# Optimization experiments

Measured on AMD Instinct MI355X. Metric: run time of the kernel, lower is better.

The kernel has to match this reference:

```python
import jax, jax.numpy as jnp
import numpy as np

N = 200000   # nodes
E = 500000   # edges
B = 4096     # batch of events
K = 20       # temporal neighbors
M = 100000   # pending raw messages
D = 128      # node feat / embedding dim
DT = 128     # time encoding dim (= D in TGN)
DM = 128     # memory dim
MSG = 128    # message dim
RAW = 2 * DM + D + DT   # 512 raw message dim
HID = RAW // 2          # 256 mlp hidden
HEADS = 2
QD = D + DT             # 256 attention query dim (= MHA embed_dim)
KD = D + DT + D         # 384 attention key dim (neigh feat + time + edge feat)
DH = QD // HEADS


def setup_inputs() -> dict:
    key = jax.random.key(0)
    ks = jax.random.split(key, 40)
    f = lambda i, shape, s=0.05: jax.random.normal(ks[i], shape, jnp.float32) * s
    ri = lambda i, shape, hi: jax.random.randint(ks[i], shape, 0, hi, jnp.int32)
    return {
        # event batch (int constants)
        'src_nodes': ri(0, (B,), N), 'dst_nodes': ri(1, (B,), N), 'neg_nodes': ri(2, (B,), N),
        'edge_times': ri(3, (B,), 1000000),
        # temporal neighbor lists for the 3B query nodes (neighbor_finder output)
        'neighbors': ri(4, (3 * B, K), N),
        'neighbor_edge_idxs': ri(5, (3 * B, K), E),
        'neighbor_edge_times': ri(6, (3 * B, K), 1000000),
        # pending raw message events ('last' aggregator picks last per node)
        'msg_src': ri(7, (M,), N), 'msg_dst': ri(8, (M,), N),
        'msg_eidx': ri(9, (M,), E), 'msg_t': ri(10, (M,), 1000000),
        'last_update': ri(11, (N,), 500000),
        # learned params / state (floats)
        'node_feats': f(12, (N, D)), 'edge_feats': f(13, (E, D)), 'memory': f(14, (N, DM)),
        'time_w': f(15, (DT,), 1.0), 'time_b': f(16, (DT,), 1.0),
        'msg_W1': f(17, (HID, RAW)), 'msg_b1': f(18, (HID,)),
        'msg_W2': f(19, (MSG, HID)), 'msg_b2': f(20, (MSG,)),
        'gru_Wi': f(21, (3 * DM, MSG)), 'gru_Wh': f(22, (3 * DM, DM)),
        'gru_bi': f(23, (3 * DM,)), 'gru_bh': f(24, (3 * DM,)),
        'Wq': f(25, (QD, QD)), 'bq': f(26, (QD,)),
        'Wk': f(27, (QD, KD)), 'bk': f(28, (QD,)),
        'Wv': f(29, (QD, KD)), 'bv': f(30, (QD,)),
        'Wo': f(31, (QD, QD)), 'bo': f(32, (QD,)),
        'mW1': f(33, (D, QD + D)), 'mb1': f(34, (D,)),
        'mW2': f(35, (D, D)), 'mb2': f(36, (D,)),
    }


def _time_enc(t, w, b):
    # TimeEncode: cos(t * w + b); t [...], out [..., DT]
    return jnp.cos(t[..., None] * w + b)


def _forward(node_feats, edge_feats, memory, time_w, time_b,
             msg_W1, msg_b1, msg_W2, msg_b2,
             gru_Wi, gru_Wh, gru_bi, gru_bh,
             Wq, bq, Wk, bk, Wv, bv, Wo, bo, mW1, mb1, mW2, mb2,
             src_nodes, dst_nodes, neg_nodes, edge_times,
             neighbors, neighbor_edge_idxs, neighbor_edge_times,
             msg_src, msg_dst, msg_eidx, msg_t, last_update):
    # ---- 1. get_updated_memory: 'last' aggregator + mlp message fn + GRU ----
    pos = jnp.arange(M, dtype=jnp.int32)
    last_pos = jnp.full((N,), -1, jnp.int32).at[msg_src].max(pos)  # last msg per node
    has_msg = last_pos >= 0
    idx = jnp.maximum(last_pos, 0)
    s, d = msg_src[idx], msg_dst[idx]
    e, t = msg_eidx[idx], msg_t[idx]
    dt = (t - last_update[s]).astype(jnp.float32)
    raw = jnp.concatenate([memory[s], memory[d], edge_feats[e],
                           _time_enc(dt, time_w, time_b)], axis=-1)  # [N, RAW]
    h1 = jax.nn.relu(raw @ msg_W1.T + msg_b1)
    msg = h1 @ msg_W2.T + msg_b2                                    # [N, MSG]
    # torch GRUCell (gate order r, z, n)
    gi = msg @ gru_Wi.T + gru_bi
    gh = memory @ gru_Wh.T + gru_bh
    ir, iz, inn = jnp.split(gi, 3, axis=-1)
    hr, hz, hn = jnp.split(gh, 3, axis=-1)
    r = jax.nn.sigmoid(ir + hr)
    z = jax.nn.sigmoid(iz + hz)
    n = jnp.tanh(inn + r * hn)
    new_mem = (1.0 - z) * n + z * memory
    mem_upd = jnp.where(has_msg[:, None], new_mem, memory)          # [N, DM]

    # ---- 2. graph-attention embedding (1 layer) over temporal neighbors ----
    nodes = jnp.concatenate([src_nodes, dst_nodes, neg_nodes])      # [3B]
    ts = jnp.tile(edge_times, 3).astype(jnp.float32)                # [3B]
    src_feat = mem_upd[nodes] + node_feats[nodes]                   # [3B, D]
    q_in = jnp.concatenate([src_feat,
                            _time_enc(jnp.zeros_like(ts), time_w, time_b)], -1)  # [3B, QD]
    pad_mask = neighbors == 0                                       # TGN: id 0 = padding
    n_feat = mem_upd[neighbors] + node_feats[neighbors]             # [3B, K, D]
    dt_n = ts[:, None] - neighbor_edge_times.astype(jnp.float32)
    k_in = jnp.concatenate([n_feat, _time_enc(dt_n, time_w, time_b),
                            edge_feats[neighbor_edge_idxs]], -1)    # [3B, K, KD]
    q = (q_in @ Wq.T + bq).reshape(-1, HEADS, DH)                   # [3B, H, DH]
    k = (k_in @ Wk.T + bk).reshape(-1, K, HEADS, DH)
    v = (k_in @ Wv.T + bv).reshape(-1, K, HEADS, DH)
    scores = jnp.einsum('bhd,bkhd->bhk', q, k) / jnp.sqrt(jnp.float32(DH))
    scores = jnp.where(pad_mask[:, None, :], -1e9, scores)
    attn = jax.nn.softmax(scores, axis=-1)                          # [3B, H, K]
    ctx = jnp.einsum('bhk,bkhd->bhd', attn, v).reshape(-1, QD)
    attn_out = ctx @ Wo.T + bo                                      # [3B, QD]
    all_masked = jnp.all(pad_mask, axis=-1)
    attn_out = jnp.where(all_masked[:, None], 0.0, attn_out)
    # MergeLayer(attn_out, src_feat)
    h = jax.nn.relu(jnp.concatenate([attn_out, src_feat], -1) @ mW1.T + mb1)
    emb = h @ mW2.T + mb2                                           # [3B, D]
    return emb.reshape(3, B, D)  # (source, destination, negative) embeddings


def reference(src_nodes, dst_nodes, neg_nodes, edge_times, neighbors,
              neighbor_edge_idxs, neighbor_edge_times, msg_src, msg_dst,
              msg_eidx, msg_t, last_update, node_feats, edge_feats, memory,
              time_w, time_b, msg_W1, msg_b1, msg_W2, msg_b2, gru_Wi, gru_Wh,
              gru_bi, gru_bh, Wq, bq, Wk, bk, Wv, bv, Wo, bo, mW1, mb1, mW2, mb2):
    return _forward(node_feats, edge_feats, memory, time_w, time_b,
                    msg_W1, msg_b1, msg_W2, msg_b2,
                    gru_Wi, gru_Wh, gru_bi, gru_bh,
                    Wq, bq, Wk, bk, Wv, bv, Wo, bo, mW1, mb1, mW2, mb2,
                    src_nodes, dst_nodes, neg_nodes, edge_times,
                    neighbors, neighbor_edge_idxs, neighbor_edge_times,
                    msg_src, msg_dst, msg_eidx, msg_t, last_update)
```

## Files before the change

kernel.cpp:

```cpp
#include <hip/hip_runtime.h>
#include <math.h>

#define NN 200000
#define EEDGE 500000
#define BB 4096
#define KK 20
#define MM 100000
#define Q3 (3*BB)
#define NBLK ((NN + 255) / 256)

typedef _Float16 __attribute__((ext_vector_type(8))) f16x8;
typedef _Float16 __attribute__((ext_vector_type(4))) f16x4;
typedef float __attribute__((ext_vector_type(4))) f32x4;

#define MFMA16(a,b,c) __builtin_amdgcn_mfma_f32_16x16x32_f16(a,b,c,0,0,0)

__device__ __forceinline__ float fast_cos(float a) {
    double ad = (double)a * 0.15915494309189535;
    double fr = ad - floor(ad);
    return __builtin_amdgcn_cosf((float)fr);
}

__device__ __forceinline__ float tenc(float dt, float w, float b) {
    float p = __fmul_rn(dt, w);
    float a = __fadd_rn(p, b);
    return fast_cos(a);
}

__device__ __forceinline__ float fsigm(float x) {
    return __builtin_amdgcn_rcpf(1.f + __expf(-x));
}
__device__ __forceinline__ float ftanh(float x) {
    return 1.f - 2.f * __builtin_amdgcn_rcpf(1.f + __expf(2.f * x));
}

__device__ __forceinline__ f32x4 z4() {
    f32x4 v; v[0] = 0.f; v[1] = 0.f; v[2] = 0.f; v[3] = 0.f; return v;
}

__global__ void k_init(int* lastpos, int* inv, char* mask) {
    int i = blockIdx.x * 256 + threadIdx.x;
    if (i < NN) { lastpos[i] = -1; inv[i] = -1; mask[i] = 0; }
}

__global__ void k_scatter(const int* __restrict__ msg_src, int* __restrict__ lastpos) {
    int i = blockIdx.x * 256 + threadIdx.x;
    if (i < MM) atomicMax(&lastpos[msg_src[i]], i);
}

__global__ void k_mark(const int* __restrict__ src_nodes, const int* __restrict__ dst_nodes,
                       const int* __restrict__ neg_nodes, const int* __restrict__ neighbors,
                       char* __restrict__ mask) {
    int i = blockIdx.x * 256 + threadIdx.x;
    if (i < Q3) {
        int node = (i < BB) ? src_nodes[i] : (i < 2 * BB) ? dst_nodes[i - BB] : neg_nodes[i - 2 * BB];
        mask[node] = 1;
    } else {
        int e = i - Q3;
        if (e < Q3 * KK) mask[neighbors[e]] = 1;
    }
}

__global__ void k_count(const int* __restrict__ lastpos, int* __restrict__ bcnt) {
    int n = blockIdx.x * 256 + threadIdx.x;
    int flag = (n < NN && lastpos[n] >= 0) ? 1 : 0;
    unsigned long long m = __ballot(flag != 0);
    __shared__ int wc[4];
    int wave = threadIdx.x >> 6, lane = threadIdx.x & 63;
    if (lane == 0) wc[wave] = __popcll(m);
    __syncthreads();
    if (threadIdx.x == 0) bcnt[blockIdx.x] = wc[0] + wc[1] + wc[2] + wc[3];
}

__global__ void k_scan(const int* __restrict__ bcnt, int* __restrict__ boff,
                       int* __restrict__ count) {
    __shared__ int s[NBLK];
    int t = threadIdx.x;
    for (int i = t; i < NBLK; i += 256) s[i] = bcnt[i];
    __syncthreads();
    if (t == 0) {
        int acc = 0;
        for (int i = 0; i < NBLK; i++) { int v = s[i]; s[i] = acc; acc += v; }
        *count = acc;
    }
    __syncthreads();
    for (int i = t; i < NBLK; i += 256) boff[i] = s[i];
}

__global__ void k_fill(const int* __restrict__ lastpos, const int* __restrict__ boff,
                       int* __restrict__ comp, int* __restrict__ inv) {
    int n = blockIdx.x * 256 + threadIdx.x;
    int flag = (n < NN && lastpos[n] >= 0) ? 1 : 0;
    unsigned long long m = __ballot(flag != 0);
    __shared__ int wc[4];
    int wave = threadIdx.x >> 6, lane = threadIdx.x & 63;
    if (lane == 0) wc[wave] = __popcll(m);
    __syncthreads();
    int base = boff[blockIdx.x];
    for (int i = 0; i < wave; i++) base += wc[i];
    int rank = __popcll(m & ((1ull << lane) - 1));
    if (flag) {
        int pos = base + rank;
        comp[pos] = n;
        inv[n] = pos;
    }
}

__global__ void k_prep(const float* __restrict__ Wq, const float* __restrict__ bq,
                       const float* __restrict__ time_b, float* __restrict__ bq2) {
    __shared__ float cte[128];
    int t = threadIdx.x;
    if (t < 128) cte[t] = fast_cos(time_b[t]);
    __syncthreads();
    float acc = bq[t];
    #pragma unroll 4
    for (int d = 0; d < 128; d++)
        acc += Wq[(size_t)t * 256 + 128 + d] * cte[d];
    bq2[t] = acc;
}

__global__ void k_cvtw(const float* __restrict__ W1, const float* __restrict__ W2,
                       const float* __restrict__ Wi, const float* __restrict__ Wh,
                       const float* __restrict__ Wq, const float* __restrict__ Wv,
                       const float* __restrict__ Wo, const float* __restrict__ mW1,
                       const float* __restrict__ mW2, const float* __restrict__ Wk,
                       _Float16* __restrict__ dst) {
    int f = blockIdx.x * 256 + threadIdx.x;
    if (f >= 77824) return;
    const float* src; int dstoff, K, ldb, lf, tr = -1;
    if      (f < 16384) { src = W1;  dstoff = 0;      K = 512; ldb = 512; lf = f; }
    else if (f < 20480) { src = W2;  dstoff = 131072; K = 256; ldb = 256; lf = f - 16384; }
    else if (f < 26624) { src = Wi;  dstoff = 163840; K = 128; ldb = 128; lf = f - 20480; }
    else if (f < 32768) { src = Wh;  dstoff = 212992; K = 128; ldb = 128; lf = f - 26624; }
    else if (f < 36864) { src = Wq;  dstoff = 262144; K = 128; ldb = 256; lf = f - 32768; }
    else if (f < 43008) { src = Wv;  dstoff = 294912; K = 384; ldb = 384; lf = f - 36864; }
    else if (f < 49152) { src = Wv + 128 * 384; dstoff = 344064; K = 384; ldb = 384; lf = f - 43008; }
    else if (f < 57344) { src = Wo;  dstoff = 393216; K = 256; ldb = 256; lf = f - 49152; }
    else if (f < 63488) { src = mW1; dstoff = 458752; K = 384; ldb = 384; lf = f - 57344; }
    else if (f < 65536) { src = mW2; dstoff = 507904; K = 128; ldb = 128; lf = f - 63488; }
    else if (f < 71680) { src = Wk;  dstoff = 524288; K = 128; ldb = 0; lf = f - 65536; tr = 0; }
    else                { src = Wk;  dstoff = 573440; K = 128; ldb = 0; lf = f - 71680; tr = 1; }
    int KS = K >> 5;
    int cgrp = lf / (KS * 64);
    int rem  = lf - cgrp * (KS * 64);
    int ks = rem >> 6, lane = rem & 63;
    int kg = lane >> 4, arow = lane & 15;
    int col = cgrp * 16 + arow;
    int k0 = ks * 32 + kg * 8;
    f16x8 h;
    if (tr < 0) {
        const float* p = src + (size_t)col * ldb + k0;
        float4 a = *(const float4*)p;
        float4 b = *(const float4*)(p + 4);
        h[0] = (_Float16)a.x; h[1] = (_Float16)a.y; h[2] = (_Float16)a.z; h[3] = (_Float16)a.w;
        h[4] = (_Float16)b.x; h[5] = (_Float16)b.y; h[6] = (_Float16)b.z; h[7] = (_Float16)b.w;
    } else {
        #pragma unroll
        for (int e = 0; e < 8; e++)
            h[e] = (_Float16)Wk[(size_t)(tr * 128 + k0 + e) * 384 + col];
    }
    *(f16x8*)(dst + dstoff + (size_t)lf * 8) = h;
}

__device__ __forceinline__ int SWA(int r, int byteofs) {
    return r * 1024 + (byteofs ^ ((r & 7) << 4));
}

__device__ __forceinline__ f16x8 ldw4(const _Float16* W, int cg, int ks, int lane) {
    return *(const f16x8*)(W + (((size_t)cg * 4 + ks) * 64 + lane) * 8);
}

__global__ __launch_bounds__(512, 2)
void k_stage1(const int* __restrict__ comp, const int* __restrict__ count,
              const int* __restrict__ lastpos,
              const int* __restrict__ msg_dst, const int* __restrict__ msg_eidx,
              const int* __restrict__ msg_t, const int* __restrict__ last_update,
              const float* __restrict__ memory, const float* __restrict__ edge_feats,
              const float* __restrict__ time_w, const float* __restrict__ time_b,
              const _Float16* __restrict__ W1h, const float* __restrict__ b1,
              const _Float16* __restrict__ W2h, const float* __restrict__ b2,
              const _Float16* __restrict__ Wih, const _Float16* __restrict__ Whh,
              const float* __restrict__ bi, const float* __restrict__ bh,
              _Float16* __restrict__ new_mem)
{
    __shared__ char rawb[64 * 1024];
    __shared__ int sn[64], sd[64], se[64];
    __shared__ float sdt[64];

    int cnt = *count;
    int r0 = blockIdx.x * 64;
    if (r0 >= cnt) return;
    int tid = threadIdx.x;

    if (tid < 64) {
        int rr = r0 + tid;
        int j = (rr < cnt) ? rr : r0;
        int n = comp[j];
        int idx = lastpos[n];
        sn[tid] = n;
        sd[tid] = msg_dst[idx];
        se[tid] = msg_eidx[idx];
        sdt[tid] = (float)(msg_t[idx] - last_update[n]);
    }
    __syncthreads();

    #pragma unroll
    for (int it = 0; it < 6; it++) {
        int gi = tid + it * 512;
        int r = gi / 48, g = gi - r * 48;
        const float* src;
        if (g < 16)      src = memory + (size_t)sn[r] * 128 + g * 8;
        else if (g < 32) src = memory + (size_t)sd[r] * 128 + (g - 16) * 8;
        else             src = edge_feats + (size_t)se[r] * 128 + (g - 32) * 8;
        float4 a = *(const float4*)src;
        float4 b = *(const float4*)(src + 4);
        f16x8 h;
        h[0] = (_Float16)a.x; h[1] = (_Float16)a.y; h[2] = (_Float16)a.z; h[3] = (_Float16)a.w;
        h[4] = (_Float16)b.x; h[5] = (_Float16)b.y; h[6] = (_Float16)b.z; h[7] = (_Float16)b.w;
        *(f16x8*)(rawb + SWA(r, g * 16)) = h;
    }
    #pragma unroll
    for (int it = 0; it < 2; it++) {
        int gi = tid + it * 512;
        int r = gi >> 4, g = gi & 15;
        int c = g * 8;
        float dt = sdt[r];
        float4 w0 = *(const float4*)(time_w + c);
        float4 w1 = *(const float4*)(time_w + c + 4);
        float4 t0 = *(const float4*)(time_b + c);
        float4 t1 = *(const float4*)(time_b + c + 4);
        f16x8 h;
        h[0] = (_Float16)tenc(dt, w0.x, t0.x); h[1] = (_Float16)tenc(dt, w0.y, t0.y);
        h[2] = (_Float16)tenc(dt, w0.z, t0.z); h[3] = (_Float16)tenc(dt, w0.w, t0.w);
        h[4] = (_Float16)tenc(dt, w1.x, t1.x); h[5] = (_Float16)tenc(dt, w1.y, t1.y);
        h[6] = (_Float16)tenc(dt, w1.z, t1.z); h[7] = (_Float16)tenc(dt, w1.w, t1.w);
        *(f16x8*)(rawb + SWA(r, (48 + g) * 16)) = h;
    }
    __syncthreads();

    int wv = tid >> 6, lane = tid & 63;
    int arow = lane & 15, kg = lane >> 4;

    f32x4 acc1[2][4];
    #pragma unroll
    for (int c = 0; c < 2; c++)
        #pragma unroll
        for (int rt = 0; rt < 4; rt++) acc1[c][rt] = z4();
    for (int ks = 0; ks < 16; ks++) {
        f16x8 a[4];
        #pragma unroll
        for (int rt = 0; rt < 4; rt++)
            a[rt] = *(const f16x8*)(rawb + SWA(rt * 16 + arow, ks * 64 + kg * 16));
        #pragma unroll
        for (int c = 0; c < 2; c++) {
            f16x8 b = *(const f16x8*)(W1h + (((size_t)(wv * 2 + c) * 16 + ks) * 64 + lane) * 8);
            #pragma unroll
            for (int rt = 0; rt < 4; rt++)
                acc1[c][rt] = MFMA16(a[rt], b, acc1[c][rt]);
        }
    }
    __syncthreads();

    #pragma unroll
    for (int c = 0; c < 2; c++) {
        int col = (wv * 2 + c) * 16 + arow;
        float bb = b1[col];
        #pragma unroll
        for (int rt = 0; rt < 4; rt++)
            #pragma unroll
            for (int rg = 0; rg < 4; rg++) {
                int row = rt * 16 + kg * 4 + rg;
                float v = fmaxf(acc1[c][rt][rg] + bb, 0.f);
                *(_Float16*)(rawb + SWA(row, 384 + col * 2)) = (_Float16)v;
            }
    }
    __syncthreads();

    f32x4 acc2[4];
    #pragma unroll
    for (int rt = 0; rt < 4; rt++) acc2[rt] = z4();
    for (int ks = 0; ks < 8; ks++) {
        f16x8 b = *(const f16x8*)(W2h + (((size_t)wv * 8 + ks) * 64 + lane) * 8);
        #pragma unroll
        for (int rt = 0; rt < 4; rt++) {
            f16x8 a = *(const f16x8*)(rawb + SWA(rt * 16 + arow, 384 + ks * 64 + kg * 16));
            acc2[rt] = MFMA16(a, b, acc2[rt]);
        }
    }
    __syncthreads();

    {
        int col = wv * 16 + arow;
        float bb = b2[col];
        #pragma unroll
        for (int rt = 0; rt < 4; rt++)
            #pragma unroll
            for (int rg = 0; rg < 4; rg++) {
                int row = rt * 16 + kg * 4 + rg;
                *(_Float16*)(rawb + SWA(row, 384 + col * 2)) =
                    (_Float16)(acc2[rt][rg] + bb);
            }
    }
    __syncthreads();

    f32x4 aR[4], aZ[4], aNi[4], aNh[4];
    #pragma unroll
    for (int rt = 0; rt < 4; rt++) { aR[rt] = z4(); aZ[rt] = z4(); aNi[rt] = z4(); aNh[rt] = z4(); }
    for (int ks = 0; ks < 4; ks++) {
        f16x8 bi_ = ldw4(Wih, wv, ks, lane);
        f16x8 bh_ = ldw4(Whh, wv, ks, lane);
        #pragma unroll
        for (int rt = 0; rt < 4; rt++) {
            f16x8 m = *(const f16x8*)(rawb + SWA(rt * 16 + arow, 384 + ks * 64 + kg * 16));
            f16x8 hh = *(const f16x8*)(rawb + SWA(rt * 16 + arow, ks * 64 + kg * 16));
            aR[rt] = MFMA16(m, bi_, aR[rt]);
            aR[rt] = MFMA16(hh, bh_, aR[rt]);
        }
    }
    for (int ks = 0; ks < 4; ks++) {
        f16x8 bi_ = ldw4(Wih, 8 + wv, ks, lane);
        f16x8 bh_ = ldw4(Whh, 8 + wv, ks, lane);
        #pragma unroll
        for (int rt = 0; rt < 4; rt++) {
            f16x8 m = *(const f16x8*)(rawb + SWA(rt * 16 + arow, 384 + ks * 64 + kg * 16));
            f16x8 hh = *(const f16x8*)(rawb + SWA(rt * 16 + arow, ks * 64 + kg * 16));
            aZ[rt] = MFMA16(m, bi_, aZ[rt]);
            aZ[rt] = MFMA16(hh, bh_, aZ[rt]);
        }
    }
    for (int ks = 0; ks < 4; ks++) {
        f16x8 bi_ = ldw4(Wih, 16 + wv, ks, lane);
        f16x8 bh_ = ldw4(Whh, 16 + wv, ks, lane);
        #pragma unroll
        for (int rt = 0; rt < 4; rt++) {
            f16x8 m = *(const f16x8*)(rawb + SWA(rt * 16 + arow, 384 + ks * 64 + kg * 16));
            f16x8 hh = *(const f16x8*)(rawb + SWA(rt * 16 + arow, ks * 64 + kg * 16));
            aNi[rt] = MFMA16(m, bi_, aNi[rt]);
            aNh[rt] = MFMA16(hh, bh_, aNh[rt]);
        }
    }

    {
        int col = wv * 16 + arow;
        float bir = bi[col],        bhr = bh[col];
        float biz = bi[128 + col],  bhz = bh[128 + col];
        float bin_ = bi[256 + col], bhn_ = bh[256 + col];
        #pragma unroll
        for (int rt = 0; rt < 4; rt++)
            #pragma unroll
            for (int rg = 0; rg < 4; rg++) {
                int row = rt * 16 + kg * 4 + rg;
                int rr = r0 + row;
                if (rr < cnt) {
                    float r_ = fsigm(aR[rt][rg] + bir + bhr);
                    float zg = fsigm(aZ[rt][rg] + biz + bhz);
                    float ng = ftanh(aNi[rt][rg] + bin_ + r_ * (aNh[rt][rg] + bhn_));
                    float om = (float)*(const _Float16*)(rawb + SWA(row, col * 2));
                    new_mem[(size_t)rr * 128 + col] = (_Float16)((1.f - zg) * ng + zg * om);
                }
            }
    }
}

__global__ __launch_bounds__(256)
void k_feat(const int* __restrict__ inv, const char* __restrict__ mask,
            const _Float16* __restrict__ new_mem,
            const float* __restrict__ memory, const float* __restrict__ node_feats,
            _Float16* __restrict__ feat)
{
    int idx = blockIdx.x * 256 + threadIdx.x;
    if (idx >= NN * 16) return;
    int n = idx >> 4, g = idx & 15;
    if (!mask[n]) return;
    int c = g * 8;
    int iv = inv[n];
    float4 n0 = *(const float4*)(node_feats + (size_t)n * 128 + c);
    float4 n1 = *(const float4*)(node_feats + (size_t)n * 128 + c + 4);
    f16x8 o;
    if (iv >= 0) {
        f16x8 mv = *(const f16x8*)(new_mem + (size_t)iv * 128 + c);
        o[0] = (_Float16)((float)mv[0] + n0.x); o[1] = (_Float16)((float)mv[1] + n0.y);
        o[2] = (_Float16)((float)mv[2] + n0.z); o[3] = (_Float16)((float)mv[3] + n0.w);
        o[4] = (_Float16)((float)mv[4] + n1.x); o[5] = (_Float16)((float)mv[5] + n1.y);
        o[6] = (_Float16)((float)mv[6] + n1.z); o[7] = (_Float16)((float)mv[7] + n1.w);
    } else {
        float4 m0 = *(const float4*)(memory + (size_t)n * 128 + c);
        float4 m1 = *(const float4*)(memory + (size_t)n * 128 + c + 4);
        o[0] = (_Float16)(m0.x + n0.x); o[1] = (_Float16)(m0.y + n0.y);
        o[2] = (_Float16)(m0.z + n0.z); o[3] = (_Float16)(m0.w + n0.w);
        o[4] = (_Float16)(m1.x + n1.x); o[5] = (_Float16)(m1.y + n1.y);
        o[6] = (_Float16)(m1.z + n1.z); o[7] = (_Float16)(m1.w + n1.w);
    }
    *(f16x8*)(feat + (size_t)n * 128 + c) = o;
}

__global__ __launch_bounds__(512, 2)
void k2b(const int* __restrict__ src_nodes, const int* __restrict__ dst_nodes,
         const int* __restrict__ neg_nodes, const _Float16* __restrict__ feat,
         const _Float16* __restrict__ WqLh, const float* __restrict__ bq2,
         const _Float16* __restrict__ Wkth,
         _Float16* __restrict__ sfeat, _Float16* __restrict__ qk_ws)
{
    __shared__ char lds[24 * 1024];
    __shared__ int snode[32];
    int tid = threadIdx.x;
    int r0 = blockIdx.x * 32;

    if (tid < 32) {
        int q = r0 + tid;
        snode[tid] = (q < BB) ? src_nodes[q] : (q < 2 * BB) ? dst_nodes[q - BB] : neg_nodes[q - 2 * BB];
    }
    __syncthreads();

    {
        int r = tid >> 4, g = tid & 15;
        f16x8 v = *(const f16x8*)(feat + (size_t)snode[r] * 128 + g * 8);
        *(f16x8*)(&lds[r * 256 + ((g * 16) ^ ((r & 7) << 4))]) = v;
        *(f16x8*)(sfeat + (size_t)(r0 + r) * 128 + g * 8) = v;
    }
    __syncthreads();

    int wv = tid >> 6, lane = tid & 63;
    int arow = lane & 15, kg = lane >> 4;

    f32x4 acc[2][2];
    #pragma unroll
    for (int c = 0; c < 2; c++) { acc[c][0] = z4(); acc[c][1] = z4(); }
    for (int ks = 0; ks < 4; ks++) {
        f16x8 a0 = *(const f16x8*)(&lds[arow * 256 + ((ks * 64 + kg * 16) ^ ((arow & 7) << 4))]);
        f16x8 a1 = *(const f16x8*)(&lds[(16 + arow) * 256 + ((ks * 64 + kg * 16) ^ ((arow & 7) << 4))]);
        #pragma unroll
        for (int c = 0; c < 2; c++) {
            f16x8 b = *(const f16x8*)(WqLh + (((size_t)(wv * 2 + c) * 4 + ks) * 64 + lane) * 8);
            acc[c][0] = MFMA16(a0, b, acc[c][0]);
            acc[c][1] = MFMA16(a1, b, acc[c][1]);
        }
    }
    #pragma unroll
    for (int c = 0; c < 2; c++) {
        int col = (wv * 2 + c) * 16 + arow;
        float bb = bq2[col];
        #pragma unroll
        for (int rt = 0; rt < 2; rt++)
            #pragma unroll
            for (int rg = 0; rg < 4; rg++) {
                int row = rt * 16 + kg * 4 + rg;
                *(_Float16*)(&lds[8192 + row * 512 + ((col * 2) ^ ((row & 7) << 4))]) =
                    (_Float16)(acc[c][rt][rg] + bb);
            }
    }
    __syncthreads();

    int h = wv >> 2;
    f32x4 acc2[6][2];
    #pragma unroll
    for (int c = 0; c < 6; c++) { acc2[c][0] = z4(); acc2[c][1] = z4(); }
    for (int ks = 0; ks < 4; ks++) {
        f16x8 a0 = *(const f16x8*)(&lds[8192 + arow * 512 +
                    ((h * 256 + ks * 64 + kg * 16) ^ ((arow & 7) << 4))]);
        f16x8 a1 = *(const f16x8*)(&lds[8192 + (16 + arow) * 512 +
                    ((h * 256 + ks * 64 + kg * 16) ^ ((arow & 7) << 4))]);
        #pragma unroll
        for (int c = 0; c < 6; c++) {
            int cgh = (wv & 3) * 6 + c;
            f16x8 b = *(const f16x8*)(Wkth + (size_t)h * 49152 +
                       (((size_t)cgh * 4 + ks) * 64 + lane) * 8);
            acc2[c][0] = MFMA16(a0, b, acc2[c][0]);
            acc2[c][1] = MFMA16(a1, b, acc2[c][1]);
        }
    }
    #pragma unroll
    for (int c = 0; c < 6; c++) {
        int cgh = (wv & 3) * 6 + c;
        int col = h * 384 + cgh * 16 + arow;
        #pragma unroll
        for (int rt = 0; rt < 2; rt++)
            #pragma unroll
            for (int rg = 0; rg < 4; rg++) {
                int row = rt * 16 + kg * 4 + rg;
                qk_ws[(size_t)(r0 + row) * 768 + col] = (_Float16)acc2[c][rt][rg];
            }
    }
}

template<int KD, int NFRAG, bool RELU>
__global__ __launch_bounds__(256, 4)
void k_gemm(const _Float16* __restrict__ A, int lda, int a_ys,
            const _Float16* __restrict__ B, int b_ys,
            const float* __restrict__ bias, int bias_ys,
            _Float16* __restrict__ C, int ldc, int c_ys,
            float* __restrict__ C32,
            const int* __restrict__ rowmask)
{
    constexpr int ROWB = KD * 2;
    __shared__ char As[32 * ROWB];
    int tid = threadIdx.x;
    int r0 = blockIdx.x * 32;
    int aoff = blockIdx.y * a_ys;
    const _Float16* Bp = B + (size_t)blockIdx.y * b_ys;
    int coff = blockIdx.y * c_ys;

    #pragma unroll
    for (int t = 0; t < (32 * KD / 8) / 256; t++) {
        int gi = tid + t * 256;
        int r = gi / (KD / 8), g = gi % (KD / 8);
        f16x8 v = *(const f16x8*)(A + (size_t)(r0 + r) * lda + aoff + g * 8);
        *(f16x8*)(&As[r * ROWB + ((g * 16) ^ ((r & 7) << 4))]) = v;
    }
    __syncthreads();

    int wv = tid >> 6, lane = tid & 63;
    int arow = lane & 15, kg = lane >> 4;
    f32x4 acc[NFRAG][2];
    #pragma unroll
    for (int c = 0; c < NFRAG; c++) { acc[c][0] = z4(); acc[c][1] = z4(); }

    #pragma unroll
    for (int ks = 0; ks < KD / 32; ks++) {
        f16x8 a0 = *(const f16x8*)(&As[arow * ROWB + ((ks * 64 + kg * 16) ^ ((arow & 7) << 4))]);
        f16x8 a1 = *(const f16x8*)(&As[(16 + arow) * ROWB + ((ks * 64 + kg * 16) ^ ((arow & 7) << 4))]);
        #pragma unroll
        for (int c = 0; c < NFRAG; c++) {
            f16x8 b = *(const f16x8*)(Bp +
                (((size_t)(wv * NFRAG + c) * (KD / 32) + ks) * 64 + lane) * 8);
            acc[c][0] = MFMA16(a0, b, acc[c][0]);
            acc[c][1] = MFMA16(a1, b, acc[c][1]);
        }
    }

    #pragma unroll
    for (int c = 0; c < NFRAG; c++) {
        int cg = (wv * NFRAG + c) * 16 + arow;
        float bb = bias ? bias[blockIdx.y * bias_ys + cg] : 0.f;
        #pragma unroll
        for (int rt = 0; rt < 2; rt++)
            #pragma unroll
            for (int rg = 0; rg < 4; rg++) {
                int grow = r0 + rt * 16 + kg * 4 + rg;
                float v = acc[c][rt][rg] + bb;
                if (RELU) v = fmaxf(v, 0.f);
                if (rowmask && rowmask[grow]) v = 0.f;
                if (C)   C[(size_t)grow * ldc + coff + cg] = (_Float16)v;
                if (C32) C32[(size_t)grow * ldc + coff + cg] = v;
            }
    }
}

__global__ __launch_bounds__(256)
void k2d(const int* __restrict__ neighbors, const int* __restrict__ nb_eidx,
         const int* __restrict__ nb_et, const int* __restrict__ edge_times,
         const _Float16* __restrict__ feat,
         const float* __restrict__ edge_feats, const float* __restrict__ time_w,
         const float* __restrict__ time_b,
         _Float16* __restrict__ qk_wsum, int* __restrict__ allm)
{
    int tid = threadIdx.x;
    int qi = blockIdx.x * 4 + (tid >> 6);
    int lane = tid & 63;
    int h = lane >> 5, l32 = lane & 31;
    int c0 = l32 * 4;

    float4 tw = *(const float4*)(time_w + c0);
    float4 tb = *(const float4*)(time_b + c0);

    const _Float16* qkp = qk_wsum + (size_t)qi * 768 + h * 384;
    f16x4 t0 = *(const f16x4*)(qkp + c0);
    f16x4 t1 = *(const f16x4*)(qkp + 128 + c0);
    f16x4 t2 = *(const f16x4*)(qkp + 256 + c0);
    float qk0[4], qk1[4], qk2[4];
    #pragma unroll
    for (int t = 0; t < 4; t++) { qk0[t] = (float)t0[t]; qk1[t] = (float)t1[t]; qk2[t] = (float)t2[t]; }

    float ts = (float)edge_times[qi & (BB - 1)];
    float m_run = -3.0e38f, l_run = 0.f;
    float w0[4] = {0,0,0,0}, w1[4] = {0,0,0,0}, w2[4] = {0,0,0,0};
    int anyv = 0;
    const float inv_sqrt = 0.08838834764831845f;

    int base = qi * KK;
    int nb_c = neighbors[base];
    int ei_c = nb_eidx[base];
    int et_c = nb_et[base];
    f16x4 fv;
    float4 ef;
    {
        fv = *(const f16x4*)(feat + (size_t)nb_c * 128 + c0);
        ef = *(const float4*)(edge_feats + (size_t)ei_c * 128 + c0);
    }

    for (int j = 0; j < KK; j++) {
        int nb_n = 0, ei_n = 0, et_n = 0;
        f16x4 fv_n = {0,0,0,0};
        float4 ef_n = {0,0,0,0};
        if (j + 1 < KK) {
            nb_n = neighbors[base + j + 1];
            ei_n = nb_eidx[base + j + 1];
            et_n = nb_et[base + j + 1];
            fv_n = *(const f16x4*)(feat + (size_t)nb_n * 128 + c0);
            ef_n = *(const float4*)(edge_feats + (size_t)ei_n * 128 + c0);
        }

        float dtf = ts - (float)et_c;
        anyv |= (nb_c != 0);
        float k0[4] = { (float)fv[0], (float)fv[1], (float)fv[2], (float)fv[3] };
        float k1[4] = { tenc(dtf, tw.x, tb.x), tenc(dtf, tw.y, tb.y),
                        tenc(dtf, tw.z, tb.z), tenc(dtf, tw.w, tb.w) };
        float k2[4] = { ef.x, ef.y, ef.z, ef.w };

        float sp = 0.f;
        #pragma unroll
        for (int t = 0; t < 4; t++)
            sp += qk0[t] * k0[t] + qk1[t] * k1[t] + qk2[t] * k2[t];
        sp += __shfl_xor(sp, 1, 32);
        sp += __shfl_xor(sp, 2, 32);
        sp += __shfl_xor(sp, 4, 32);
        sp += __shfl_xor(sp, 8, 32);
        sp += __shfl_xor(sp, 16, 32);

        float s = sp * inv_sqrt;
        if (nb_c == 0) s = -1e9f;
        float m_new = fmaxf(m_run, s);
        float sc = __expf(m_run - m_new);
        float p = __expf(s - m_new);
        l_run = l_run * sc + p;
        #pragma unroll
        for (int t = 0; t < 4; t++) {
            w0[t] = w0[t] * sc + p * k0[t];
            w1[t] = w1[t] * sc + p * k1[t];
            w2[t] = w2[t] * sc + p * k2[t];
        }
        m_run = m_new;

        nb_c = nb_n; ei_c = ei_n; et_c = et_n;
        fv = fv_n; ef = ef_n;
    }

    float linv = __builtin_amdgcn_rcpf(l_run);
    _Float16* wp = qk_wsum + (size_t)qi * 768 + h * 384;
    f16x4 o0, o1, o2;
    #pragma unroll
    for (int t = 0; t < 4; t++) {
        o0[t] = (_Float16)(w0[t] * linv);
        o1[t] = (_Float16)(w1[t] * linv);
        o2[t] = (_Float16)(w2[t] * linv);
    }
    *(f16x4*)(wp + c0) = o0;
    *(f16x4*)(wp + 128 + c0) = o1;
    *(f16x4*)(wp + 256 + c0) = o2;
    if (lane == 0) allm[qi] = anyv ? 0 : 1;
}

__global__ __launch_bounds__(256, 2)
void k2t2(const _Float16* __restrict__ ctx, const _Float16* __restrict__ sfeat,
          const _Float16* __restrict__ Woh, const float* __restrict__ bo,
          const _Float16* __restrict__ mW1h, const float* __restrict__ mb1,
          const _Float16* __restrict__ mW2h, const float* __restrict__ mb2,
          const int* __restrict__ allm, float* __restrict__ out)
{
    __shared__ char lds[48 * 1024];
    int tid = threadIdx.x;
    int r0 = blockIdx.x * 32;

    #pragma unroll
    for (int t = 0; t < 4; t++) {
        int gi = tid + t * 256;
        int r = gi >> 5, g = gi & 31;
        f16x8 v = *(const f16x8*)(ctx + (size_t)(r0 + r) * 256 + g * 8);
        *(f16x8*)(&lds[r * 512 + ((g * 16) ^ ((r & 7) << 4))]) = v;
    }
    __syncthreads();

    int wv = tid >> 6, lane = tid & 63;
    int arow = lane & 15, kg = lane >> 4;

    f32x4 acc[4][2];
    #pragma unroll
    for (int c = 0; c < 4; c++) { acc[c][0] = z4(); acc[c][1] = z4(); }
    for (int ks = 0; ks < 8; ks++) {
        f16x8 a0 = *(const f16x8*)(&lds[arow * 512 + ((ks * 64 + kg * 16) ^ ((arow & 7) << 4))]);
        f16x8 a1 = *(const f16x8*)(&lds[(16 + arow) * 512 + ((ks * 64 + kg * 16) ^ ((arow & 7) << 4))]);
        #pragma unroll
        for (int c = 0; c < 4; c++) {
            f16x8 b = *(const f16x8*)(Woh + (((size_t)(wv * 4 + c) * 8 + ks) * 64 + lane) * 8);
            acc[c][0] = MFMA16(a0, b, acc[c][0]);
            acc[c][1] = MFMA16(a1, b, acc[c][1]);
        }
    }
    #pragma unroll
    for (int c = 0; c < 4; c++) {
        int col = (wv * 4 + c) * 16 + arow;
        float bb = bo[col];
        #pragma unroll
        for (int rt = 0; rt < 2; rt++)
            #pragma unroll
            for (int rg = 0; rg < 4; rg++) {
                int row = rt * 16 + kg * 4 + rg;
                float v = allm[r0 + row] ? 0.f : (acc[c][rt][rg] + bb);
                *(_Float16*)(&lds[16384 + row * 768 + ((col * 2) ^ ((row & 7) << 4))]) = (_Float16)v;
            }
    }
    #pragma unroll
    for (int t = 0; t < 2; t++) {
        int gi = tid + t * 256;
        int r = gi >> 4, g = gi & 15;
        f16x8 v = *(const f16x8*)(sfeat + (size_t)(r0 + r) * 128 + g * 8);
        *(f16x8*)(&lds[16384 + r * 768 + ((512 + g * 16) ^ ((r & 7) << 4))]) = v;
    }
    __syncthreads();

    f32x4 acc2[2][2];
    #pragma unroll
    for (int c = 0; c < 2; c++) { acc2[c][0] = z4(); acc2[c][1] = z4(); }
    for (int ks = 0; ks < 12; ks++) {
        f16x8 a0 = *(const f16x8*)(&lds[16384 + arow * 768 + ((ks * 64 + kg * 16) ^ ((arow & 7) << 4))]);
        f16x8 a1 = *(const f16x8*)(&lds[16384 + (16 + arow) * 768 + ((ks * 64 + kg * 16) ^ ((arow & 7) << 4))]);
        #pragma unroll
        for (int c = 0; c < 2; c++) {
            f16x8 b = *(const f16x8*)(mW1h + (((size_t)(wv * 2 + c) * 12 + ks) * 64 + lane) * 8);
            acc2[c][0] = MFMA16(a0, b, acc2[c][0]);
            acc2[c][1] = MFMA16(a1, b, acc2[c][1]);
        }
    }
    #pragma unroll
    for (int c = 0; c < 2; c++) {
        int col = (wv * 2 + c) * 16 + arow;
        float bb = mb1[col];
        #pragma unroll
        for (int rt = 0; rt < 2; rt++)
            #pragma unroll
            for (int rg = 0; rg < 4; rg++) {
                int row = rt * 16 + kg * 4 + rg;
                float v = fmaxf(acc2[c][rt][rg] + bb, 0.f);
                *(_Float16*)(&lds[40960 + row * 256 + ((col * 2) ^ ((row & 7) << 4))]) = (_Float16)v;
            }
    }
    __syncthreads();

    f32x4 acc3[2][2];
    #pragma unroll
    for (int c = 0; c < 2; c++) { acc3[c][0] = z4(); acc3[c][1] = z4(); }
    for (int ks = 0; ks < 4; ks++) {
        f16x8 a0 = *(const f16x8*)(&lds[40960 + arow * 256 + ((ks * 64 + kg * 16) ^ ((arow & 7) << 4))]);
        f16x8 a1 = *(const f16x8*)(&lds[40960 + (16 + arow) * 256 + ((ks * 64 + kg * 16) ^ ((arow & 7) << 4))]);
        #pragma unroll
        for (int c = 0; c < 2; c++) {
            f16x8 b = *(const f16x8*)(mW2h + (((size_t)(wv * 2 + c) * 4 + ks) * 64 + lane) * 8);
            acc3[c][0] = MFMA16(a0, b, acc3[c][0]);
            acc3[c][1] = MFMA16(a1, b, acc3[c][1]);
        }
    }
    #pragma unroll
    for (int c = 0; c < 2; c++) {
        int col = (wv * 2 + c) * 16 + arow;
        float bb = mb2[col];
        #pragma unroll
        for (int rt = 0; rt < 2; rt++)
            #pragma unroll
            for (int rg = 0; rg < 4; rg++) {
                int row = rt * 16 + kg * 4 + rg;
                out[(size_t)(r0 + row) * 128 + col] = acc3[c][rt][rg] + bb;
            }
    }
}

extern "C" void kernel_launch(void* const* d_in, const int* in_sizes, int n_in,
                              void* d_out, int out_size, void* d_ws, size_t ws_size,
                              hipStream_t stream) {
    (void)in_sizes; (void)n_in; (void)out_size; (void)ws_size;
    const int* src_nodes  = (const int*)d_in[0];
    const int* dst_nodes  = (const int*)d_in[1];
    const int* neg_nodes  = (const int*)d_in[2];
    const int* edge_times = (const int*)d_in[3];
    const int* neighbors  = (const int*)d_in[4];
    const int* nb_eidx    = (const int*)d_in[5];
    const int* nb_et      = (const int*)d_in[6];
    const int* msg_src    = (const int*)d_in[7];
    const int* msg_dst    = (const int*)d_in[8];
    const int* msg_eidx   = (const int*)d_in[9];
    const int* msg_t      = (const int*)d_in[10];
    const int* last_update= (const int*)d_in[11];
    const float* node_feats = (const float*)d_in[12];
    const float* edge_feats = (const float*)d_in[13];
    const float* memory     = (const float*)d_in[14];
    const float* time_w = (const float*)d_in[15];
    const float* time_b = (const float*)d_in[16];
    const float* W1 = (const float*)d_in[17];
    const float* b1 = (const float*)d_in[18];
    const float* W2 = (const float*)d_in[19];
    const float* b2 = (const float*)d_in[20];
    const float* gWi = (const float*)d_in[21];
    const float* gWh = (const float*)d_in[22];
    const float* gbi = (const float*)d_in[23];
    const float* gbh = (const float*)d_in[24];
    const float* Wq = (const float*)d_in[25];
    const float* bq = (const float*)d_in[26];
    const float* Wk = (const float*)d_in[27];
    const float* bk = (const float*)d_in[28];
    const float* Wv = (const float*)d_in[29];
    const float* bv = (const float*)d_in[30];
    const float* Wo = (const float*)d_in[31];
    const float* bo = (const float*)d_in[32];
    const float* mW1 = (const float*)d_in[33];
    const float* mb1 = (const float*)d_in[34];
    const float* mW2 = (const float*)d_in[35];
    const float* mb2 = (const float*)d_in[36];
    float* out = (float*)d_out;
    (void)bk;

    char* w = (char*)d_ws;
    int* lastpos = (int*)w;
    int* inv  = lastpos + NN;
    int* comp = inv + NN;
    int* count = comp + NN;
    int* bcnt = count + 1;
    int* boff = bcnt + NBLK;
    char* mask = (char*)(boff + NBLK);
    size_t off = ((size_t)(3 * NN + 1 + 2 * NBLK) * 4 + NN + 255) & ~(size_t)255;
    _Float16* new_mem = (_Float16*)(w + off);
    size_t foff = off + (size_t)MM * 128 * 2;
    _Float16* feat = (_Float16*)(w + foff);
    size_t woff = foff + (size_t)NN * 128 * 2;

    _Float16* Hpool = (_Float16*)(w + woff);
    _Float16* W1h  = Hpool;
    _Float16* W2h  = Hpool + 131072;
    _Float16* Wih  = Hpool + 163840;
    _Float16* Whh  = Hpool + 212992;
    _Float16* WqLh = Hpool + 262144;
    _Float16* Wvh  = Hpool + 294912;
    _Float16* Woh  = Hpool + 393216;
    _Float16* mW1h = Hpool + 458752;
    _Float16* mW2h = Hpool + 507904;
    _Float16* Wkth = Hpool + 524288;
    float* bq2 = (float*)(Hpool + 622592);
    size_t boff2 = woff + (size_t)622592 * 2 + 1024;

    _Float16* ctx   = (_Float16*)(w + boff2);
    _Float16* qk_ws = ctx + (size_t)Q3 * 256;
    _Float16* sfeat = qk_ws + (size_t)Q3 * 768;
    int* allm       = (int*)(sfeat + (size_t)Q3 * 128);

    k_init<<<dim3(NBLK), dim3(256), 0, stream>>>(lastpos, inv, mask);
    k_scatter<<<dim3((MM + 255) / 256), dim3(256), 0, stream>>>(msg_src, lastpos);
    k_mark<<<dim3((Q3 + Q3 * KK + 255) / 256), dim3(256), 0, stream>>>(
        src_nodes, dst_nodes, neg_nodes, neighbors, mask);
    k_count<<<dim3(NBLK), dim3(256), 0, stream>>>(lastpos, bcnt);
    k_scan<<<dim3(1), dim3(256), 0, stream>>>(bcnt, boff, count);
    k_fill<<<dim3(NBLK), dim3(256), 0, stream>>>(lastpos, boff, comp, inv);
    k_cvtw<<<dim3(304), dim3(256), 0, stream>>>(W1, W2, gWi, gWh, Wq, Wv, Wo, mW1, mW2, Wk, Hpool);
    k_prep<<<dim3(1), dim3(256), 0, stream>>>(Wq, bq, time_b, bq2);
    k_stage1<<<dim3((MM + 63) / 64), dim3(512), 0, stream>>>(
        comp, count, lastpos, msg_dst, msg_eidx, msg_t, last_update,
        memory, edge_feats, time_w, time_b,
        W1h, b1, W2h, b2, Wih, Whh, gbi, gbh, new_mem);
    k_feat<<<dim3(NN * 16 / 256), dim3(256), 0, stream>>>(
        inv, mask, new_mem, memory, node_feats, feat);

    k2b<<<dim3(Q3 / 32), dim3(512), 0, stream>>>(
        src_nodes, dst_nodes, neg_nodes, feat, WqLh, bq2, Wkth, sfeat, qk_ws);
    k2d<<<dim3(Q3 / 4), dim3(256), 0, stream>>>(
        neighbors, nb_eidx, nb_et, edge_times, feat,
        edge_feats, time_w, time_b, qk_ws, allm);
    k_gemm<384, 2, false><<<dim3(Q3 / 32, 2), dim3(256), 0, stream>>>(
        qk_ws, 768, 384, Wvh, 49152, bv, 128, ctx, 256, 128, nullptr, nullptr);
    k2t2<<<dim3(Q3 / 32), dim3(256), 0, stream>>>(
        ctx, sfeat, Woh, bo, mW1h, mb1, mW2h, mb2, allm, out);
}
```

Baseline: 284.4 us.

## Shrink stage1 row tile to 48 and fold small prep kernels into neighbors

The stage1 fused MLP+GRU kernel now processes 48 rows per block instead of 64. This shrinks LDS use to 48 KB and lowers accumulator register pressure, and the launch bound hint rises from 2 to 6 blocks per CU so more blocks can be resident. The inv initialization moves from k_init into k_fill, and the bq2 precompute kernel becomes an extra block of k_cvtw, removing one launch and one memory pass. The trade-off is more blocks and more redundant weight loads per row, since each weight fragment is now amortized over fewer rows.

```diff
diff --git a/kernel.cpp b/kernel.cpp
--- a/kernel.cpp
+++ b/kernel.cpp
@@ -8,6 +8,7 @@
 #define MM 100000
 #define Q3 (3*BB)
 #define NBLK ((NN + 255) / 256)
+#define S1R 48
 
 typedef _Float16 __attribute__((ext_vector_type(8))) f16x8;
 typedef _Float16 __attribute__((ext_vector_type(4))) f16x4;
@@ -38,9 +39,9 @@
     f32x4 v; v[0] = 0.f; v[1] = 0.f; v[2] = 0.f; v[3] = 0.f; return v;
 }
 
-__global__ void k_init(int* lastpos, int* inv, char* mask) {
+__global__ void k_init(int* lastpos, char* mask) {
     int i = blockIdx.x * 256 + threadIdx.x;
-    if (i < NN) { lastpos[i] = -1; inv[i] = -1; mask[i] = 0; }
+    if (i < NN) { lastpos[i] = -1; mask[i] = 0; }
 }
 
 __global__ void k_scatter(const int* __restrict__ msg_src, int* __restrict__ lastpos) {
@@ -99,24 +100,11 @@
     int base = boff[blockIdx.x];
     for (int i = 0; i < wave; i++) base += wc[i];
     int rank = __popcll(m & ((1ull << lane) - 1));
-    if (flag) {
+    if (n < NN) {
         int pos = base + rank;
-        comp[pos] = n;
-        inv[n] = pos;
-    }
-}
-
-__global__ void k_prep(const float* __restrict__ Wq, const float* __restrict__ bq,
-                       const float* __restrict__ time_b, float* __restrict__ bq2) {
-    __shared__ float cte[128];
-    int t = threadIdx.x;
-    if (t < 128) cte[t] = fast_cos(time_b[t]);
-    __syncthreads();
-    float acc = bq[t];
-    #pragma unroll 4
-    for (int d = 0; d < 128; d++)
-        acc += Wq[(size_t)t * 256 + 128 + d] * cte[d];
-    bq2[t] = acc;
+        if (flag) comp[pos] = n;
+        inv[n] = flag ? pos : -1;
+    }
 }
 
 __global__ void k_cvtw(const float* __restrict__ W1, const float* __restrict__ W2,
@@ -124,7 +112,20 @@
                        const float* __restrict__ Wq, const float* __restrict__ Wv,
                        const float* __restrict__ Wo, const float* __restrict__ mW1,
                        const float* __restrict__ mW2, const float* __restrict__ Wk,
-                       _Float16* __restrict__ dst) {
+                       const float* __restrict__ bq, const float* __restrict__ time_b,
+                       _Float16* __restrict__ dst, float* __restrict__ bq2) {
+    if (blockIdx.x == 304) {
+        __shared__ float cte[128];
+        int t = threadIdx.x;
+        if (t < 128) cte[t] = fast_cos(time_b[t]);
+        __syncthreads();
+        float acc = bq[t];
+        #pragma unroll 4
+        for (int d = 0; d < 128; d++)
+            acc += Wq[(size_t)t * 256 + 128 + d] * cte[d];
+        bq2[t] = acc;
+        return;
+    }
     int f = blockIdx.x * 256 + threadIdx.x;
     if (f >= 77824) return;
     const float* src; int dstoff, K, ldb, lf, tr = -1;
@@ -170,7 +171,7 @@
     return *(const f16x8*)(W + (((size_t)cg * 4 + ks) * 64 + lane) * 8);
 }
 
-__global__ __launch_bounds__(512, 2)
+__global__ __launch_bounds__(512, 6)
 void k_stage1(const int* __restrict__ comp, const int* __restrict__ count,
               const int* __restrict__ lastpos,
               const int* __restrict__ msg_dst, const int* __restrict__ msg_eidx,
@@ -183,16 +184,16 @@
               const float* __restrict__ bi, const float* __restrict__ bh,
               _Float16* __restrict__ new_mem)
 {
-    __shared__ char rawb[64 * 1024];
-    __shared__ int sn[64], sd[64], se[64];
-    __shared__ float sdt[64];
+    __shared__ char rawb[S1R * 1024];
+    __shared__ int sn[S1R], sd[S1R], se[S1R];
+    __shared__ float sdt[S1R];
 
     int cnt = *count;
-    int r0 = blockIdx.x * 64;
+    int r0 = blockIdx.x * S1R;
     if (r0 >= cnt) return;
     int tid = threadIdx.x;
 
-    if (tid < 64) {
+    if (tid < S1R) {
         int rr = r0 + tid;
         int j = (rr < cnt) ? rr : r0;
         int n = comp[j];
@@ -204,9 +205,7 @@
     }
     __syncthreads();
 
-    #pragma unroll
-    for (int it = 0; it < 6; it++) {
-        int gi = tid + it * 512;
+    for (int gi = tid; gi < S1R * 48; gi += 512) {
         int r = gi / 48, g = gi - r * 48;
         const float* src;
         if (g < 16)      src = memory + (size_t)sn[r] * 128 + g * 8;
@@ -219,9 +218,7 @@
         h[4] = (_Float16)b.x; h[5] = (_Float16)b.y; h[6] = (_Float16)b.z; h[7] = (_Float16)b.w;
         *(f16x8*)(rawb + SWA(r, g * 16)) = h;
     }
-    #pragma unroll
-    for (int it = 0; it < 2; it++) {
-        int gi = tid + it * 512;
+    for (int gi = tid; gi < S1R * 16; gi += 512) {
         int r = gi >> 4, g = gi & 15;
         int c = g * 8;
         float dt = sdt[r];
@@ -241,21 +238,21 @@
     int wv = tid >> 6, lane = tid & 63;
     int arow = lane & 15, kg = lane >> 4;
 
-    f32x4 acc1[2][4];
+    f32x4 acc1[2][3];
     #pragma unroll
     for (int c = 0; c < 2; c++)
         #pragma unroll
-        for (int rt = 0; rt < 4; rt++) acc1[c][rt] = z4();
+        for (int rt = 0; rt < 3; rt++) acc1[c][rt] = z4();
     for (int ks = 0; ks < 16; ks++) {
-        f16x8 a[4];
-        #pragma unroll
-        for (int rt = 0; rt < 4; rt++)
+        f16x8 a[3];
+        #pragma unroll
+        for (int rt = 0; rt < 3; rt++)
             a[rt] = *(const f16x8*)(rawb + SWA(rt * 16 + arow, ks * 64 + kg * 16));
         #pragma unroll
         for (int c = 0; c < 2; c++) {
             f16x8 b = *(const f16x8*)(W1h + (((size_t)(wv * 2 + c) * 16 + ks) * 64 + lane) * 8);
             #pragma unroll
-            for (int rt = 0; rt < 4; rt++)
+            for (int rt = 0; rt < 3; rt++)
                 acc1[c][rt] = MFMA16(a[rt], b, acc1[c][rt]);
         }
     }
@@ -266,7 +263,7 @@
         int col = (wv * 2 + c) * 16 + arow;
         float bb = b1[col];
         #pragma unroll
-        for (int rt = 0; rt < 4; rt++)
+        for (int rt = 0; rt < 3; rt++)
             #pragma unroll
             for (int rg = 0; rg < 4; rg++) {
                 int row = rt * 16 + kg * 4 + rg;
@@ -276,13 +273,13 @@
     }
     __syncthreads();
 
-    f32x4 acc2[4];
-    #pragma unroll
-    for (int rt = 0; rt < 4; rt++) acc2[rt] = z4();
+    f32x4 acc2[3];
+    #pragma unroll
+    for (int rt = 0; rt < 3; rt++) acc2[rt] = z4();
     for (int ks = 0; ks < 8; ks++) {
         f16x8 b = *(const f16x8*)(W2h + (((size_t)wv * 8 + ks) * 64 + lane) * 8);
         #pragma unroll
-        for (int rt = 0; rt < 4; rt++) {
+        for (int rt = 0; rt < 3; rt++) {
             f16x8 a = *(const f16x8*)(rawb + SWA(rt * 16 + arow, 384 + ks * 64 + kg * 16));
             acc2[rt] = MFMA16(a, b, acc2[rt]);
         }
@@ -293,7 +290,7 @@
         int col = wv * 16 + arow;
         float bb = b2[col];
         #pragma unroll
-        for (int rt = 0; rt < 4; rt++)
+        for (int rt = 0; rt < 3; rt++)
             #pragma unroll
             for (int rg = 0; rg < 4; rg++) {
                 int row = rt * 16 + kg * 4 + rg;
@@ -303,14 +300,14 @@
     }
     __syncthreads();
 
-    f32x4 aR[4], aZ[4], aNi[4], aNh[4];
-    #pragma unroll
-    for (int rt = 0; rt < 4; rt++) { aR[rt] = z4(); aZ[rt] = z4(); aNi[rt] = z4(); aNh[rt] = z4(); }
+    f32x4 aR[3], aZ[3], aNi[3], aNh[3];
+    #pragma unroll
+    for (int rt = 0; rt < 3; rt++) { aR[rt] = z4(); aZ[rt] = z4(); aNi[rt] = z4(); aNh[rt] = z4(); }
     for (int ks = 0; ks < 4; ks++) {
         f16x8 bi_ = ldw4(Wih, wv, ks, lane);
         f16x8 bh_ = ldw4(Whh, wv, ks, lane);
         #pragma unroll
-        for (int rt = 0; rt < 4; rt++) {
+        for (int rt = 0; rt < 3; rt++) {
             f16x8 m = *(const f16x8*)(rawb + SWA(rt * 16 + arow, 384 + ks * 64 + kg * 16));
             f16x8 hh = *(const f16x8*)(rawb + SWA(rt * 16 + arow, ks * 64 + kg * 16));
             aR[rt] = MFMA16(m, bi_, aR[rt]);
@@ -321,7 +318,7 @@
         f16x8 bi_ = ldw4(Wih, 8 + wv, ks, lane);
         f16x8 bh_ = ldw4(Whh, 8 + wv, ks, lane);
         #pragma unroll
-        for (int rt = 0; rt < 4; rt++) {
+        for (int rt = 0; rt < 3; rt++) {
             f16x8 m = *(const f16x8*)(rawb + SWA(rt * 16 + arow, 384 + ks * 64 + kg * 16));
             f16x8 hh = *(const f16x8*)(rawb + SWA(rt * 16 + arow, ks * 64 + kg * 16));
             aZ[rt] = MFMA16(m, bi_, aZ[rt]);
@@ -332,7 +329,7 @@
         f16x8 bi_ = ldw4(Wih, 16 + wv, ks, lane);
         f16x8 bh_ = ldw4(Whh, 16 + wv, ks, lane);
         #pragma unroll
-        for (int rt = 0; rt < 4; rt++) {
+        for (int rt = 0; rt < 3; rt++) {
             f16x8 m = *(const f16x8*)(rawb + SWA(rt * 16 + arow, 384 + ks * 64 + kg * 16));
             f16x8 hh = *(const f16x8*)(rawb + SWA(rt * 16 + arow, ks * 64 + kg * 16));
             aNi[rt] = MFMA16(m, bi_, aNi[rt]);
@@ -346,7 +343,7 @@
         float biz = bi[128 + col],  bhz = bh[128 + col];
         float bin_ = bi[256 + col], bhn_ = bh[256 + col];
         #pragma unroll
-        for (int rt = 0; rt < 4; rt++)
+        for (int rt = 0; rt < 3; rt++)
             #pragma unroll
             for (int rg = 0; rg < 4; rg++) {
                 int row = rt * 16 + kg * 4 + rg;
@@ -840,16 +837,16 @@
     _Float16* sfeat = qk_ws + (size_t)Q3 * 768;
     int* allm       = (int*)(sfeat + (size_t)Q3 * 128);
 
-    k_init<<<dim3(NBLK), dim3(256), 0, stream>>>(lastpos, inv, mask);
+    k_init<<<dim3(NBLK), dim3(256), 0, stream>>>(lastpos, mask);
     k_scatter<<<dim3((MM + 255) / 256), dim3(256), 0, stream>>>(msg_src, lastpos);
     k_mark<<<dim3((Q3 + Q3 * KK + 255) / 256), dim3(256), 0, stream>>>(
         src_nodes, dst_nodes, neg_nodes, neighbors, mask);
     k_count<<<dim3(NBLK), dim3(256), 0, stream>>>(lastpos, bcnt);
     k_scan<<<dim3(1), dim3(256), 0, stream>>>(bcnt, boff, count);
     k_fill<<<dim3(NBLK), dim3(256), 0, stream>>>(lastpos, boff, comp, inv);
-    k_cvtw<<<dim3(304), dim3(256), 0, stream>>>(W1, W2, gWi, gWh, Wq, Wv, Wo, mW1, mW2, Wk, Hpool);
-    k_prep<<<dim3(1), dim3(256), 0, stream>>>(Wq, bq, time_b, bq2);
-    k_stage1<<<dim3((MM + 63) / 64), dim3(512), 0, stream>>>(
+    k_cvtw<<<dim3(305), dim3(256), 0, stream>>>(
+        W1, W2, gWi, gWh, Wq, Wv, Wo, mW1, mW2, Wk, bq, time_b, Hpool, bq2);
+    k_stage1<<<dim3((MM + S1R - 1) / S1R), dim3(512), 0, stream>>>(
         comp, count, lastpos, msg_dst, msg_eidx, msg_t, last_update,
         memory, edge_feats, time_w, time_b,
         W1h, b1, W2h, b2, Wih, Whh, gbi, gbh, new_mem);
```

Measured after the change: 336.8 us. 1.18x slower.
